# Performance work log

Measured on AMD Instinct MI355X. Metric: run time of the kernel, lower is better.

The kernel has to match this reference:

```python
import jax, jax.numpy as jnp
import numpy as np

N, E = 50000, 1600000
F_IN, EDGE_DIM, HID, HEADS, NCLS = 64, 16, 128, 4, 40
C = HID // HEADS  # per-head dim = 32


def setup_inputs() -> dict:
    key = jax.random.key(0)
    ks = jax.random.split(key, 20)
    s = 0.1
    inp = {
        'x': jax.random.normal(ks[0], (N, F_IN), jnp.float32),
        'edge_index': jax.random.randint(ks[1], (2, E), 0, N, jnp.int64),
        'edge_attr': jax.random.normal(ks[2], (E, EDGE_DIM), jnp.float32),
        # layer 1 params
        'W1': jax.random.normal(ks[3], (HID, F_IN), jnp.float32) * s,
        'as1': jax.random.normal(ks[4], (HEADS, C), jnp.float32) * s,
        'ad1': jax.random.normal(ks[5], (HEADS, C), jnp.float32) * s,
        'ae1': jax.random.normal(ks[6], (HEADS, C), jnp.float32) * s,
        'We1': jax.random.normal(ks[7], (HID, EDGE_DIM), jnp.float32) * s,
        'b1': jnp.zeros((HID,), jnp.float32),
        # layer 2 params
        'W2': jax.random.normal(ks[8], (HID, HID), jnp.float32) * s,
        'as2': jax.random.normal(ks[9], (HEADS, C), jnp.float32) * s,
        'ad2': jax.random.normal(ks[10], (HEADS, C), jnp.float32) * s,
        'ae2': jax.random.normal(ks[11], (HEADS, C), jnp.float32) * s,
        'We2': jax.random.normal(ks[12], (HID, EDGE_DIM), jnp.float32) * s,
        'b2': jnp.zeros((HID,), jnp.float32),
        # final classifier
        'Wlin': jax.random.normal(ks[13], (NCLS, HID), jnp.float32) * s,
        'blin': jnp.zeros((NCLS,), jnp.float32),
    }
    return inp


def gat_conv(x, src, dst, eattr, W, a_s, a_d, a_e, We, b):
    """PyG GATConv (concat=True, add_self_loops=True, fill_value='mean'), eval mode."""
    n = x.shape[0]
    H, Cd = a_s.shape
    h = (x @ W.T).reshape(n, H, Cd)  # [N,H,C]
    # self-loop edge_attr = per-destination mean of incoming edge_attr
    cnt = jax.ops.segment_sum(jnp.ones((dst.shape[0],), eattr.dtype), dst, num_segments=n)
    mean_ea = jax.ops.segment_sum(eattr, dst, num_segments=n) / jnp.maximum(cnt, 1.0)[:, None]
    loops = jnp.arange(n, dtype=src.dtype)
    s_idx = jnp.concatenate([src, loops])
    d_idx = jnp.concatenate([dst, loops])
    ea = jnp.concatenate([eattr, mean_ea], axis=0)  # [E+N, edge_dim]
    e = (ea @ We.T).reshape(-1, H, Cd)
    # edge-wise attention logits
    alpha = (h * a_s).sum(-1)[s_idx] + (h * a_d).sum(-1)[d_idx] + (e * a_e).sum(-1)  # [E+N,H]
    alpha = jax.nn.leaky_relu(alpha, 0.2)
    # segment softmax over destination neighborhoods (every node has a self-loop)
    amax = jax.ops.segment_max(alpha, d_idx, num_segments=n)
    ex = jnp.exp(alpha - amax[d_idx])
    den = jax.ops.segment_sum(ex, d_idx, num_segments=n)
    coef = ex / (den[d_idx] + 1e-16)
    out = jax.ops.segment_sum(h[s_idx] * coef[:, :, None], d_idx, num_segments=n)
    return out.reshape(n, H * Cd) + b


def reference(x, edge_index, edge_attr, W1, as1, ad1, ae1, We1, b1,
              W2, as2, ad2, ae2, We2, b2, Wlin, blin):
    src, dst = edge_index[0], edge_index[1]
    h = jax.nn.relu(gat_conv(x, src, dst, edge_attr, W1, as1, ad1, ae1, We1, b1))
    h = jax.nn.relu(gat_conv(h, src, dst, edge_attr, W2, as2, ad2, ae2, We2, b2))
    logits = h @ Wlin.T + blin
    return jax.nn.log_softmax(logits, axis=1)
```

## Files before the change

### kernel.cpp

```cpp
#include <hip/hip_runtime.h>
#include <hip/hip_bf16.h>
#include <math.h>


#define CHUNK 2048

typedef __attribute__((ext_vector_type(8))) short short8;
typedef __attribute__((ext_vector_type(4))) float floatx4;
typedef __attribute__((ext_vector_type(2))) float floatx2;

__device__ __forceinline__ unsigned short f2bf(float f) {
  unsigned u = __float_as_uint(f);
  unsigned r = u + 0x7FFFu + ((u >> 16) & 1u);
  return (unsigned short)(r >> 16);
}
__device__ __forceinline__ float bf2f(unsigned short b) {
  return __uint_as_float(((unsigned)b) << 16);
}

__global__ __launch_bounds__(256) void alphaseq_kernel(const float* __restrict__ ea,
                                                       const float* __restrict__ ae1,
                                                       const float* __restrict__ We1,
                                                       const float* __restrict__ ae2,
                                                       const float* __restrict__ We2,
                                                       const int* __restrict__ dst,
                                                       int* __restrict__ bucketCnt,
                                                       uint2* __restrict__ tA1,
                                                       uint2* __restrict__ tA2,
                                                       int E, int NB) {
  __shared__ float wa[128];
  __shared__ int hist[512];
  const int tid = threadIdx.x;
  hist[tid] = 0;
  hist[tid + 256] = 0;
  if (tid < 128) {
    const float* aev = (tid < 64) ? ae1 : ae2;
    const float* Wev = (tid < 64) ? We1 : We2;
    const int h = (tid >> 4) & 3;
    const int d = tid & 15;
    float s = 0.f;
#pragma unroll
    for (int c = 0; c < 32; ++c) s += aev[h * 32 + c] * Wev[(h * 32 + c) * 16 + d];
    wa[tid] = s;
  }
  __syncthreads();
  const int e0 = blockIdx.x * CHUNK, e1 = min(e0 + CHUNK, E);
  for (int e = e0 + tid; e < e1; e += 256) {
    atomicAdd(&hist[dst[e] >> 7], 1);
    const float4* p = (const float4*)(ea + (size_t)e * 16);
    float4 q0 = p[0], q1 = p[1], q2 = p[2], q3 = p[3];
    float v[16] = {q0.x, q0.y, q0.z, q0.w, q1.x, q1.y, q1.z, q1.w,
                   q2.x, q2.y, q2.z, q2.w, q3.x, q3.y, q3.z, q3.w};
    unsigned short rr[8];
#pragma unroll
    for (int h = 0; h < 8; ++h) {
      float s = 0.f;
#pragma unroll
      for (int d = 0; d < 16; ++d) s += v[d] * wa[h * 16 + d];
      rr[h] = f2bf(s);
    }
    uint2 lo, hi;
    lo.x = ((unsigned)rr[1] << 16) | rr[0];
    lo.y = ((unsigned)rr[3] << 16) | rr[2];
    hi.x = ((unsigned)rr[5] << 16) | rr[4];
    hi.y = ((unsigned)rr[7] << 16) | rr[6];
    tA1[e] = lo;
    tA2[e] = hi;
  }
  __syncthreads();
  for (int i = tid; i < NB; i += 256)
    if (hist[i]) atomicAdd(&bucketCnt[i], hist[i]);
}

__global__ __launch_bounds__(512) void scanB_kernel(const int* __restrict__ bucketCnt,
                                                    int* __restrict__ bucketOffs,
                                                    int* __restrict__ bucketPos,
                                                    int* __restrict__ offs,
                                                    int NB, int N, int E) {
  __shared__ int sc[512];
  const int tid = threadIdx.x;
  const int v = (tid < NB) ? bucketCnt[tid] : 0;
  sc[tid] = v;
  __syncthreads();
  for (int off = 1; off < 512; off <<= 1) {
    int t = (tid >= off) ? sc[tid - off] : 0;
    __syncthreads();
    sc[tid] += t;
    __syncthreads();
  }
  const int excl = sc[tid] - v;
  if (tid < NB) { bucketOffs[tid] = excl; bucketPos[tid] = excl; }
  if (tid == 0) { bucketOffs[NB] = E; offs[N] = E; }
}

__global__ __launch_bounds__(512) void partB_kernel(const int* __restrict__ src,
                                                    const int* __restrict__ dst,
                                                    const uint2* __restrict__ tA1,
                                                    const uint2* __restrict__ tA2,
                                                    int* __restrict__ bucketPos,
                                                    int4* __restrict__ binned16,
                                                    int* __restrict__ binned4,
                                                    unsigned char* __restrict__ dlArr,
                                                    int E, int NB) {
  __shared__ int hist[512], sc[512], lbase[513], gbase[512], lcnt[512];
  __shared__ int4 stg16[CHUNK];
  __shared__ int stg4[CHUNK];
  __shared__ unsigned char stg1[CHUNK];
  const int tid = threadIdx.x;
  const int e0 = blockIdx.x * CHUNK;
  const int e1 = min(e0 + CHUNK, E);
  hist[tid] = 0; lcnt[tid] = 0;
  __syncthreads();
  for (int e = e0 + tid; e < e1; e += 512) atomicAdd(&hist[dst[e] >> 7], 1);
  __syncthreads();
  sc[tid] = hist[tid];
  __syncthreads();
  for (int off = 1; off < 512; off <<= 1) {
    int t = (tid >= off) ? sc[tid - off] : 0;
    __syncthreads();
    sc[tid] += t;
    __syncthreads();
  }
  lbase[tid + 1] = sc[tid];
  if (tid == 0) lbase[0] = 0;
  if (tid < NB && hist[tid] > 0) gbase[tid] = atomicAdd(&bucketPos[tid], hist[tid]);
  __syncthreads();
  for (int e = e0 + tid; e < e1; e += 512) {
    const int d = dst[e];
    const int b = d >> 7;
    const int lr = atomicAdd(&lcnt[b], 1);
    const uint2 a1 = tA1[e];
    const uint2 a2 = tA2[e];
    int4 v;
    v.x = (src[e] & 0xFFFF) | ((d & 127) << 16);
    v.y = (int)a1.x;
    v.z = (int)a1.y;
    v.w = (int)a2.x;
    const int sp = lbase[b] + lr;
    stg16[sp] = v;
    stg4[sp] = (int)a2.y;
    stg1[sp] = (unsigned char)(d & 127);
  }
  __syncthreads();
  const int total = e1 - e0;
  for (int t = tid; t < total; t += 512) {
    int lo = 0, hi = 511;
    while (lo < hi) {
      int mid = (lo + hi + 1) >> 1;
      if (lbase[mid] <= t) lo = mid; else hi = mid - 1;
    }
    const int g = gbase[lo] + (t - lbase[lo]);
    binned16[g] = stg16[t];
    binned4[g] = stg4[t];
    dlArr[g] = stg1[t];
  }
}

__global__ __launch_bounds__(256) void passC_kernel(const int4* __restrict__ binned16,
                                                    const int* __restrict__ binned4,
                                                    const unsigned char* __restrict__ dlArr,
                                                    const int* __restrict__ bucketOffs,
                                                    int* __restrict__ srcS,
                                                    uint2* __restrict__ aeS1,
                                                    uint2* __restrict__ aeS2,
                                                    int* __restrict__ offs, int N) {
  __shared__ int cnt[128], dbase[129], dpos[128];
  const int tid = threadIdx.x;
  const int b = blockIdx.x;
  const int bo = bucketOffs[b], be = bucketOffs[b + 1];
  const int m = be - bo;
  if (tid < 128) { cnt[tid] = 0; dpos[tid] = 0; }
  __syncthreads();
  for (int t = tid; t < m; t += 256) atomicAdd(&cnt[dlArr[bo + t]], 1);
  __syncthreads();
  for (int off = 1; off < 128; off <<= 1) {
    int t = (tid < 128 && tid >= (unsigned)off) ? cnt[tid - off] : 0;
    __syncthreads();
    if (tid < 128) cnt[tid] += t;
    __syncthreads();
  }
  if (tid == 0) dbase[0] = 0;
  if (tid < 128) dbase[tid + 1] = cnt[tid];
  __syncthreads();
  const int dcnt = min(128, N - (b << 7));
  if (tid < dcnt) offs[(b << 7) + tid] = bo + dbase[tid];
  for (int t = tid; t < m; t += 256) {
    const int4 v = binned16[bo + t];
    const int w4 = binned4[bo + t];
    const int dl = (v.x >> 16) & 127;
    const int p = dbase[dl] + atomicAdd(&dpos[dl], 1);
    srcS[bo + p] = v.x & 0xFFFF;
    aeS1[bo + p] = make_uint2((unsigned)v.y, (unsigned)v.z);
    aeS2[bo + p] = make_uint2((unsigned)v.w, (unsigned)w4);
  }
}

__global__ __launch_bounds__(256) void cvtall_kernel(const float* __restrict__ W1,
                                                     unsigned short* __restrict__ Wb1,
                                                     const float* __restrict__ W2,
                                                     unsigned short* __restrict__ Wb2,
                                                     const float* __restrict__ Wlin,
                                                     unsigned short* __restrict__ whi,
                                                     unsigned short* __restrict__ wlo) {
  const int n1 = 128 * 64, n2 = 128 * 128, n3 = 48 * 128;
  int i = blockIdx.x * 256 + threadIdx.x;
  if (i < n1) {
    Wb1[i] = f2bf(W1[i]);
  } else if (i < n1 + n2) {
    Wb2[i - n1] = f2bf(W2[i - n1]);
  } else if (i < n1 + n2 + n3) {
    const int j = i - n1 - n2;
    float v = (j < 40 * 128) ? Wlin[j] : 0.f;
    unsigned short h = f2bf(v);
    whi[j] = h;
    wlo[j] = f2bf(v - bf2f(h));
  }
}

#define GEMM_SCORE_EPILOGUE()                                                      \
  {                                                                                \
    const float as0 = a_s[ncol0], as1v = a_s[ncol0 + 16];                          \
    const float ad0 = a_d[ncol0], ad1v = a_d[ncol0 + 16];                          \
    _Pragma("unroll") for (int mt = 0; mt < 4; ++mt) {                             \
      _Pragma("unroll") for (int r = 0; r < 4; ++r) {                              \
        float ps = acc[mt][0][r] * as0 + acc[mt][1][r] * as1v;                     \
        float pd = acc[mt][0][r] * ad0 + acc[mt][1][r] * ad1v;                     \
        _Pragma("unroll") for (int off = 8; off; off >>= 1) {                      \
          ps += __shfl_xor(ps, off, 16);                                           \
          pd += __shfl_xor(pd, off, 16);                                           \
        }                                                                          \
        if (l15 == 0) {                                                            \
          const int row = m0 + mt * 16 + (quad << 2) + r;                          \
          if (row < n) {                                                           \
            ssc[(size_t)row * 4 + w] = ps;                                         \
            dsc[(size_t)row * 4 + w] = pd;                                         \
          }                                                                        \
        }                                                                          \
      }                                                                            \
    }                                                                              \
  }

__global__ __launch_bounds__(256) void gemm_score_f32_kernel(const float* __restrict__ X,
                                                             const unsigned short* __restrict__ Wb,
                                                             const float* __restrict__ a_s,
                                                             const float* __restrict__ a_d,
                                                             unsigned short* __restrict__ H,
                                                             float* __restrict__ ssc,
                                                             float* __restrict__ dsc,
                                                             int n) {
  const int w = threadIdx.x >> 6;
  const int lane = threadIdx.x & 63;
  const int m0 = blockIdx.x * 64;
  const int quad = lane >> 4;
  const int l15 = lane & 15;
  floatx4 acc[4][2];
#pragma unroll
  for (int mt = 0; mt < 4; ++mt)
#pragma unroll
    for (int nt = 0; nt < 2; ++nt) acc[mt][nt] = (floatx4)(0.f);

  int rowm[4];
#pragma unroll
  for (int mt = 0; mt < 4; ++mt) {
    int r = m0 + mt * 16 + l15;
    rowm[mt] = (r < n) ? r : (n - 1);
  }
  const int ncol0 = (w << 5) + l15;

#pragma unroll
  for (int kc = 0; kc < 64; kc += 32) {
    const int koff = kc + (quad << 3);
    short8 a[4], b[2];
#pragma unroll
    for (int mt = 0; mt < 4; ++mt) {
      const float* pr = X + (size_t)rowm[mt] * 64 + koff;
      float4 q0 = *(const float4*)pr;
      float4 q1 = *(const float4*)(pr + 4);
      a[mt][0] = (short)f2bf(q0.x); a[mt][1] = (short)f2bf(q0.y);
      a[mt][2] = (short)f2bf(q0.z); a[mt][3] = (short)f2bf(q0.w);
      a[mt][4] = (short)f2bf(q1.x); a[mt][5] = (short)f2bf(q1.y);
      a[mt][6] = (short)f2bf(q1.z); a[mt][7] = (short)f2bf(q1.w);
    }
#pragma unroll
    for (int nt = 0; nt < 2; ++nt)
      b[nt] = *(const short8*)(Wb + (size_t)(ncol0 + nt * 16) * 64 + koff);
#pragma unroll
    for (int mt = 0; mt < 4; ++mt)
#pragma unroll
      for (int nt = 0; nt < 2; ++nt)
        acc[mt][nt] = __builtin_amdgcn_mfma_f32_16x16x32_bf16(a[mt], b[nt], acc[mt][nt], 0, 0, 0);
  }
#pragma unroll
  for (int mt = 0; mt < 4; ++mt) {
    const int rbase = m0 + mt * 16 + (quad << 2);
#pragma unroll
    for (int nt = 0; nt < 2; ++nt) {
      const int col = ncol0 + nt * 16;
#pragma unroll
      for (int r = 0; r < 4; ++r) {
        const int row = rbase + r;
        if (row < n) H[(size_t)row * 128 + col] = f2bf(acc[mt][nt][r]);
      }
    }
  }
  GEMM_SCORE_EPILOGUE()
}

__global__ __launch_bounds__(256) void gemm_score_kernel(const unsigned short* __restrict__ X,
                                                         const unsigned short* __restrict__ Wb,
                                                         const float* __restrict__ a_s,
                                                         const float* __restrict__ a_d,
                                                         unsigned short* __restrict__ H,
                                                         float* __restrict__ ssc,
                                                         float* __restrict__ dsc,
                                                         int n, int K) {
  const int w = threadIdx.x >> 6;
  const int lane = threadIdx.x & 63;
  const int m0 = blockIdx.x * 64;
  const int quad = lane >> 4;
  const int l15 = lane & 15;
  floatx4 acc[4][2];
#pragma unroll
  for (int mt = 0; mt < 4; ++mt)
#pragma unroll
    for (int nt = 0; nt < 2; ++nt) acc[mt][nt] = (floatx4)(0.f);

  int rowm[4];
#pragma unroll
  for (int mt = 0; mt < 4; ++mt) {
    int r = m0 + mt * 16 + l15;
    rowm[mt] = (r < n) ? r : (n - 1);
  }
  const int ncol0 = (w << 5) + l15;

  for (int kc = 0; kc < K; kc += 32) {
    const int koff = kc + (quad << 3);
    short8 a[4], b[2];
#pragma unroll
    for (int mt = 0; mt < 4; ++mt)
      a[mt] = *(const short8*)(X + (size_t)rowm[mt] * K + koff);
#pragma unroll
    for (int nt = 0; nt < 2; ++nt)
      b[nt] = *(const short8*)(Wb + (size_t)(ncol0 + nt * 16) * K + koff);
#pragma unroll
    for (int mt = 0; mt < 4; ++mt)
#pragma unroll
      for (int nt = 0; nt < 2; ++nt)
        acc[mt][nt] = __builtin_amdgcn_mfma_f32_16x16x32_bf16(a[mt], b[nt], acc[mt][nt], 0, 0, 0);
  }
#pragma unroll
  for (int mt = 0; mt < 4; ++mt) {
    const int rbase = m0 + mt * 16 + (quad << 2);
#pragma unroll
    for (int nt = 0; nt < 2; ++nt) {
      const int col = ncol0 + nt * 16;
#pragma unroll
      for (int r = 0; r < 4; ++r) {
        const int row = rbase + r;
        if (row < n) H[(size_t)row * 128 + col] = f2bf(acc[mt][nt][r]);
      }
    }
  }
  GEMM_SCORE_EPILOGUE()
}

__device__ __forceinline__ float leaky02(float a) { return a > 0.f ? a : 0.2f * a; }
__device__ __forceinline__ float sel4(float4 v, int h) {
  return (h == 0) ? v.x : (h == 1) ? v.y : (h == 2) ? v.z : v.w;
}

__global__ __launch_bounds__(256) void agg_kernel(const unsigned short* __restrict__ hin,
                                                  const float* __restrict__ ssc,
                                                  const float* __restrict__ dsc,
                                                  const unsigned short* __restrict__ aeS,
                                                  const int* __restrict__ offs,
                                                  const int* __restrict__ srcS,
                                                  const float* __restrict__ bias,
                                                  unsigned short* __restrict__ hout, int n) {
  __shared__ int sbuf[4][64];
  __shared__ float pbuf[4][256];
  const int tid = threadIdx.x;
  const int wv = tid >> 6;
  const int lane = tid & 63;
  const int node = blockIdx.x * 4 + wv;
  if (node >= n) return;
  const int l32 = lane & 31;
  const int half = lane >> 5;
  const int ch4 = l32 * 4;
  const int headB = l32 >> 3;
  const float4 dv = *(const float4*)(dsc + (size_t)node * 4);
  float4 l4 = make_float4(0.f, 0.f, 0.f, 0.f);
  float4 sa = make_float4(0.f, 0.f, 0.f, 0.f);
  floatx2 acc01 = (floatx2)(0.f);
  floatx2 acc23 = (floatx2)(0.f);
  const int j0 = offs[node], j1 = offs[node + 1];

  for (int jc = j0; jc < j1; jc += 64) {
    const int len = min(64, j1 - jc);
    float4 p4 = make_float4(0.f, 0.f, 0.f, 0.f);
    int sv = 0;
    if (lane < len) {
      const int j = jc + lane;
      sv = srcS[j];
      const ushort4 aq = *(const ushort4*)(aeS + (size_t)j * 4);
      const float4 ae4 = make_float4(bf2f(aq.x), bf2f(aq.y), bf2f(aq.z), bf2f(aq.w));
      const float4 ss4 = *(const float4*)(ssc + (size_t)sv * 4);
      sa.x += ae4.x; sa.y += ae4.y; sa.z += ae4.z; sa.w += ae4.w;
      p4.x = __expf(leaky02(ss4.x + dv.x + ae4.x));
      p4.y = __expf(leaky02(ss4.y + dv.y + ae4.y));
      p4.z = __expf(leaky02(ss4.z + dv.z + ae4.z));
      p4.w = __expf(leaky02(ss4.w + dv.w + ae4.w));
    }
    sbuf[wv][lane] = sv;
    *(float4*)(&pbuf[wv][lane * 4]) = p4;
    l4.x += p4.x; l4.y += p4.y; l4.z += p4.z; l4.w += p4.w;
    int k = 0;
    for (; k + 8 <= len; k += 8) {
      int s[4];
      float p[4];
      uint2 d[4];
#pragma unroll
      for (int u = 0; u < 4; ++u) {
        const int kk = k + 2 * u + half;
        s[u] = sbuf[wv][kk];
        p[u] = pbuf[wv][kk * 4 + headB];
      }
#pragma unroll
      for (int u = 0; u < 4; ++u)
        d[u] = *(const uint2*)(hin + (size_t)s[u] * 128 + ch4);
#pragma unroll
      for (int u = 0; u < 4; ++u) {
        floatx2 p2; p2.x = p[u]; p2.y = p[u];
        floatx2 h01, h23;
        h01.x = __uint_as_float(d[u].x << 16);
        h01.y = __uint_as_float(d[u].x & 0xFFFF0000u);
        h23.x = __uint_as_float(d[u].y << 16);
        h23.y = __uint_as_float(d[u].y & 0xFFFF0000u);
        acc01 += p2 * h01;
        acc23 += p2 * h23;
      }
    }
    for (; k < len; k += 2) {
      int kk = k + half;
      if (kk < len) {
        int s = sbuf[wv][kk];
        float p = pbuf[wv][kk * 4 + headB];
        uint2 d = *(const uint2*)(hin + (size_t)s * 128 + ch4);
        floatx2 p2; p2.x = p; p2.y = p;
        floatx2 h01, h23;
        h01.x = __uint_as_float(d.x << 16);
        h01.y = __uint_as_float(d.x & 0xFFFF0000u);
        h23.x = __uint_as_float(d.y << 16);
        h23.y = __uint_as_float(d.y & 0xFFFF0000u);
        acc01 += p2 * h01;
        acc23 += p2 * h23;
      }
    }
  }

  float acc[4] = {acc01.x, acc01.y, acc23.x, acc23.y};
#pragma unroll
  for (int off = 32; off; off >>= 1) {
    sa.x += __shfl_xor(sa.x, off);
    sa.y += __shfl_xor(sa.y, off);
    sa.z += __shfl_xor(sa.z, off);
    sa.w += __shfl_xor(sa.w, off);
    l4.x += __shfl_xor(l4.x, off);
    l4.y += __shfl_xor(l4.y, off);
    l4.z += __shfl_xor(l4.z, off);
    l4.w += __shfl_xor(l4.w, off);
  }
#pragma unroll
  for (int i = 0; i < 4; ++i) acc[i] += __shfl_xor(acc[i], 32);

  const int deg = j1 - j0;
  const float invd = 1.f / fmaxf((float)deg, 1.f);
  const float ssn = ssc[(size_t)node * 4 + headB];
  const float aloop = leaky02(ssn + sel4(dv, headB) + sel4(sa, headB) * invd);
  const float pl = __expf(aloop);
  const float lF = sel4(l4, headB) + pl;
  const uint2 hd = *(const uint2*)(hin + (size_t)node * 128 + ch4);
  const float hv0 = __uint_as_float(hd.x << 16);
  const float hv1 = __uint_as_float(hd.x & 0xFFFF0000u);
  const float hv2 = __uint_as_float(hd.y << 16);
  const float hv3 = __uint_as_float(hd.y & 0xFFFF0000u);
  const float inv = 1.f / (lF + 1e-16f);
  const float4 bi = *(const float4*)(bias + ch4);
  const float o0 = fmaxf((acc[0] + pl * hv0) * inv + bi.x, 0.f);
  const float o1 = fmaxf((acc[1] + pl * hv1) * inv + bi.y, 0.f);
  const float o2 = fmaxf((acc[2] + pl * hv2) * inv + bi.z, 0.f);
  const float o3 = fmaxf((acc[3] + pl * hv3) * inv + bi.w, 0.f);
  if (half == 0) {
    ushort4 o;
    o.x = f2bf(o0); o.y = f2bf(o1); o.z = f2bf(o2); o.w = f2bf(o3);
    *(ushort4*)(hout + (size_t)node * 128 + ch4) = o;
  }
}

__global__ __launch_bounds__(256) void classifier_kernel(const unsigned short* __restrict__ h,
                                                         const unsigned short* __restrict__ Whi,
                                                         const unsigned short* __restrict__ Wlo,
                                                         const float* __restrict__ blin,
                                                         float* __restrict__ out, int n) {
  const int w = threadIdx.x >> 6;
  const int lane = threadIdx.x & 63;
  const int quad = lane >> 4;
  const int l15 = lane & 15;
  const int row0 = blockIdx.x * 64 + w * 16;
  if (row0 >= n) return;
  int rowm = row0 + l15;
  if (rowm >= n) rowm = n - 1;
  floatx4 acc[3];
#pragma unroll
  for (int nt = 0; nt < 3; ++nt) acc[nt] = (floatx4)(0.f);
  const size_t hbase = (size_t)rowm * 128;
#pragma unroll
  for (int kc = 0; kc < 128; kc += 32) {
    const int koff = kc + (quad << 3);
    short8 a = *(const short8*)(h + hbase + koff);
#pragma unroll
    for (int nt = 0; nt < 3; ++nt) {
      short8 bh = *(const short8*)(Whi + (size_t)(nt * 16 + l15) * 128 + koff);
      short8 bl = *(const short8*)(Wlo + (size_t)(nt * 16 + l15) * 128 + koff);
      acc[nt] = __builtin_amdgcn_mfma_f32_16x16x32_bf16(a, bh, acc[nt], 0, 0, 0);
      acc[nt] = __builtin_amdgcn_mfma_f32_16x16x32_bf16(a, bl, acc[nt], 0, 0, 0);
    }
  }
  const float bl0 = blin[l15];
  const float bl1 = blin[16 + l15];
  const float bl2 = (l15 < 8) ? blin[32 + l15] : 0.f;
#pragma unroll
  for (int r = 0; r < 4; ++r) {
    const int rrow = row0 + (quad << 2) + r;
    const float v0 = acc[0][r] + bl0;
    const float v1 = acc[1][r] + bl1;
    const float v2 = (l15 < 8) ? (acc[2][r] + bl2) : -INFINITY;
    float m = fmaxf(v0, fmaxf(v1, v2));
#pragma unroll
    for (int off = 8; off; off >>= 1) m = fmaxf(m, __shfl_xor(m, off, 16));
    const float e2 = (l15 < 8) ? __expf(v2 - m) : 0.f;
    float s = __expf(v0 - m) + __expf(v1 - m) + e2;
#pragma unroll
    for (int off = 8; off; off >>= 1) s += __shfl_xor(s, off, 16);
    const float ls = m + __logf(s);
    if (rrow < n) {
      float* po = out + (size_t)rrow * 40;
      po[l15] = v0 - ls;
      po[16 + l15] = v1 - ls;
      if (l15 < 8) po[32 + l15] = v2 - ls;
    }
  }
}

extern "C" void kernel_launch(void* const* d_in, const int* in_sizes, int n_in,
                              void* d_out, int out_size, void* d_ws, size_t ws_size,
                              hipStream_t stream) {
  const float* x    = (const float*)d_in[0];
  const int*   eidx = (const int*)d_in[1];
  const float* ea   = (const float*)d_in[2];
  const float* W1   = (const float*)d_in[3];
  const float* as1  = (const float*)d_in[4];
  const float* ad1  = (const float*)d_in[5];
  const float* ae1w = (const float*)d_in[6];
  const float* We1  = (const float*)d_in[7];
  const float* b1   = (const float*)d_in[8];
  const float* W2   = (const float*)d_in[9];
  const float* as2  = (const float*)d_in[10];
  const float* ad2  = (const float*)d_in[11];
  const float* ae2w = (const float*)d_in[12];
  const float* We2  = (const float*)d_in[13];
  const float* b2   = (const float*)d_in[14];
  const float* Wlin = (const float*)d_in[15];
  const float* blin = (const float*)d_in[16];
  float* out = (float*)d_out;

  const int N = in_sizes[0] / 64;
  const int E = in_sizes[1] / 2;
  const int* src = eidx;
  const int* dst = eidx + E;
  const int NB = (N + 127) >> 7;

  char* wsb = (char*)d_ws;
  size_t off = 0;
  auto alloc = [&](size_t bytes) -> void* {
    void* p = wsb + off;
    off = (off + bytes + 255) & ~(size_t)255;
    return p;
  };
  int* bucketCnt  = (int*)alloc(512 * 4);
  int* bucketOffs = (int*)alloc(513 * 4);
  int* bucketPos  = (int*)alloc(512 * 4);
  int* offs       = (int*)alloc((size_t)(N + 1) * 4);
  uint2* tA1      = (uint2*)alloc((size_t)E * 8);
  uint2* tA2      = (uint2*)alloc((size_t)E * 8);
  void* regC      = alloc((size_t)E * 16);
  int4* binned16  = (int4*)regC;
  unsigned short* hA = (unsigned short*)regC;
  int* binned4    = (int*)alloc((size_t)E * 4);
  unsigned char* dlArr = (unsigned char*)alloc((size_t)E);
  int* srcS       = (int*)alloc((size_t)E * 4);
  unsigned short* Wb1 = (unsigned short*)alloc(128 * 64 * 2);
  unsigned short* Wb2 = (unsigned short*)alloc(128 * 128 * 2);
  unsigned short* Wlh = (unsigned short*)alloc(48 * 128 * 2);
  unsigned short* Wll = (unsigned short*)alloc(48 * 128 * 2);
  float* ssc      = (float*)alloc((size_t)N * 4 * 4);
  float* dsc      = (float*)alloc((size_t)N * 4 * 4);
  unsigned short* hB = (unsigned short*)alloc((size_t)N * 128 * 2);
  uint2* aeS1 = tA1;
  uint2* aeS2 = tA2;

  const int gg = (N + 63) / 64;
  const int gs = (N + 3) / 4;
  const int gp = (E + CHUNK - 1) / CHUNK;
  const int ncvt = 128 * 64 + 128 * 128 + 48 * 128;

  hipMemsetAsync(bucketCnt, 0, 512 * 4, stream);
  alphaseq_kernel<<<gp, 256, 0, stream>>>(ea, ae1w, We1, ae2w, We2, dst, bucketCnt,
                                          tA1, tA2, E, NB);
  scanB_kernel<<<1, 512, 0, stream>>>(bucketCnt, bucketOffs, bucketPos, offs, NB, N, E);
  partB_kernel<<<gp, 512, 0, stream>>>(src, dst, tA1, tA2, bucketPos, binned16, binned4,
                                       dlArr, E, NB);
  passC_kernel<<<NB, 256, 0, stream>>>(binned16, binned4, dlArr, bucketOffs, srcS,
                                       aeS1, aeS2, offs, N);

  cvtall_kernel<<<(ncvt + 255) / 256, 256, 0, stream>>>(W1, Wb1, W2, Wb2, Wlin, Wlh, Wll);

  gemm_score_f32_kernel<<<gg, 256, 0, stream>>>(x, Wb1, as1, ad1, hA, ssc, dsc, N);
  agg_kernel<<<gs, 256, 0, stream>>>(hA, ssc, dsc, (const unsigned short*)aeS1, offs, srcS, b1, hB, N);

  gemm_score_kernel<<<gg, 256, 0, stream>>>(hB, Wb2, as2, ad2, hA, ssc, dsc, N, 128);
  agg_kernel<<<gs, 256, 0, stream>>>(hA, ssc, dsc, (const unsigned short*)aeS2, offs, srcS, b2, hB, N);

  classifier_kernel<<<gg, 256, 0, stream>>>(hB, Wlh, Wll, blin, out, N);
}
```

Before: 473.5 us.

## Stage GEMM tiles in LDS and scatter partB directly without local staging

The two score GEMM kernels now cooperatively load the A row tile and the full weight matrix into padded LDS before running the MFMA loop, instead of each lane issuing strided global loads per k-step. The fp32 input is converted to bf16 once during staging. Separately, partB drops its block-local prefix scan, shared staging buffers and binary-search copy-out, writing each edge straight to its global bucket slot. That saves LDS and synchronisation but makes the global writes scattered and uncoalesced, and edge order within a bucket now depends on atomic timing.

```diff
diff --git a/kernel.cpp b/kernel.cpp
--- a/kernel.cpp
+++ b/kernel.cpp
@@ -102,10 +102,7 @@
                                                     int* __restrict__ binned4,
                                                     unsigned char* __restrict__ dlArr,
                                                     int E, int NB) {
-  __shared__ int hist[512], sc[512], lbase[513], gbase[512], lcnt[512];
-  __shared__ int4 stg16[CHUNK];
-  __shared__ int stg4[CHUNK];
-  __shared__ unsigned char stg1[CHUNK];
+  __shared__ int hist[512], gbase[512], lcnt[512];
   const int tid = threadIdx.x;
   const int e0 = blockIdx.x * CHUNK;
   const int e1 = min(e0 + CHUNK, E);
@@ -113,22 +110,13 @@
   __syncthreads();
   for (int e = e0 + tid; e < e1; e += 512) atomicAdd(&hist[dst[e] >> 7], 1);
   __syncthreads();
-  sc[tid] = hist[tid];
-  __syncthreads();
-  for (int off = 1; off < 512; off <<= 1) {
-    int t = (tid >= off) ? sc[tid - off] : 0;
-    __syncthreads();
-    sc[tid] += t;
-    __syncthreads();
-  }
-  lbase[tid + 1] = sc[tid];
-  if (tid == 0) lbase[0] = 0;
   if (tid < NB && hist[tid] > 0) gbase[tid] = atomicAdd(&bucketPos[tid], hist[tid]);
   __syncthreads();
   for (int e = e0 + tid; e < e1; e += 512) {
     const int d = dst[e];
     const int b = d >> 7;
     const int lr = atomicAdd(&lcnt[b], 1);
+    const int g = gbase[b] + lr;
     const uint2 a1 = tA1[e];
     const uint2 a2 = tA2[e];
     int4 v;
@@ -136,23 +124,9 @@
     v.y = (int)a1.x;
     v.z = (int)a1.y;
     v.w = (int)a2.x;
-    const int sp = lbase[b] + lr;
-    stg16[sp] = v;
-    stg4[sp] = (int)a2.y;
-    stg1[sp] = (unsigned char)(d & 127);
-  }
-  __syncthreads();
-  const int total = e1 - e0;
-  for (int t = tid; t < total; t += 512) {
-    int lo = 0, hi = 511;
-    while (lo < hi) {
-      int mid = (lo + hi + 1) >> 1;
-      if (lbase[mid] <= t) lo = mid; else hi = mid - 1;
-    }
-    const int g = gbase[lo] + (t - lbase[lo]);
-    binned16[g] = stg16[t];
-    binned4[g] = stg4[t];
-    dlArr[g] = stg1[t];
+    binned16[g] = v;
+    binned4[g] = (int)a2.y;
+    dlArr[g] = (unsigned char)(d & 127);
   }
 }
 
@@ -240,6 +214,37 @@
     }                                                                              \
   }
 
+#define GEMM_MFMA_FROM_LDS(KTOT, PA, PB)                                           \
+  {                                                                                \
+    for (int kc = 0; kc < (KTOT); kc += 32) {                                      \
+      const int koff = kc + (quad << 3);                                           \
+      short8 a[4], b[2];                                                           \
+      _Pragma("unroll") for (int mt = 0; mt < 4; ++mt)                             \
+        a[mt] = *(const short8*)(&As[(mt * 16 + l15) * (PA) + koff]);              \
+      _Pragma("unroll") for (int nt = 0; nt < 2; ++nt)                             \
+        b[nt] = *(const short8*)(&Bs[(ncol0 + nt * 16) * (PB) + koff]);            \
+      _Pragma("unroll") for (int mt = 0; mt < 4; ++mt)                             \
+        _Pragma("unroll") for (int nt = 0; nt < 2; ++nt)                           \
+          acc[mt][nt] =                                                            \
+              __builtin_amdgcn_mfma_f32_16x16x32_bf16(a[mt], b[nt], acc[mt][nt],   \
+                                                      0, 0, 0);                    \
+    }                                                                              \
+  }
+
+#define GEMM_WRITE_H()                                                             \
+  {                                                                                \
+    _Pragma("unroll") for (int mt = 0; mt < 4; ++mt) {                             \
+      const int rbase = m0 + mt * 16 + (quad << 2);                                \
+      _Pragma("unroll") for (int nt = 0; nt < 2; ++nt) {                           \
+        const int col = ncol0 + nt * 16;                                           \
+        _Pragma("unroll") for (int r = 0; r < 4; ++r) {                            \
+          const int row = rbase + r;                                               \
+          if (row < n) H[(size_t)row * 128 + col] = f2bf(acc[mt][nt][r]);          \
+        }                                                                          \
+      }                                                                            \
+    }                                                                              \
+  }
+
 __global__ __launch_bounds__(256) void gemm_score_f32_kernel(const float* __restrict__ X,
                                                              const unsigned short* __restrict__ Wb,
                                                              const float* __restrict__ a_s,
@@ -248,61 +253,44 @@
                                                              float* __restrict__ ssc,
                                                              float* __restrict__ dsc,
                                                              int n) {
-  const int w = threadIdx.x >> 6;
-  const int lane = threadIdx.x & 63;
+  __shared__ unsigned short As[64 * 72];
+  __shared__ unsigned short Bs[128 * 72];
+  const int tid = threadIdx.x;
+  const int w = tid >> 6;
+  const int lane = tid & 63;
   const int m0 = blockIdx.x * 64;
   const int quad = lane >> 4;
   const int l15 = lane & 15;
+
+#pragma unroll
+  for (int it = 0; it < 4; ++it) {
+    const int idx = it * 256 + tid;
+    const int row = idx >> 4;
+    const int c4 = (idx & 15) * 4;
+    const int grow = min(m0 + row, n - 1);
+    const float4 q = *(const float4*)(X + (size_t)grow * 64 + c4);
+    unsigned short* dstp = &As[row * 72 + c4];
+    dstp[0] = f2bf(q.x); dstp[1] = f2bf(q.y); dstp[2] = f2bf(q.z); dstp[3] = f2bf(q.w);
+  }
+#pragma unroll
+  for (int it = 0; it < 4; ++it) {
+    const int idx = it * 256 + tid;
+    const int row = idx >> 3;
+    const int c8 = (idx & 7) * 8;
+    short8 v = *(const short8*)(Wb + (size_t)row * 64 + c8);
+    *(short8*)(&Bs[row * 72 + c8]) = v;
+  }
+  __syncthreads();
+
   floatx4 acc[4][2];
 #pragma unroll
   for (int mt = 0; mt < 4; ++mt)
 #pragma unroll
     for (int nt = 0; nt < 2; ++nt) acc[mt][nt] = (floatx4)(0.f);
-
-  int rowm[4];
-#pragma unroll
-  for (int mt = 0; mt < 4; ++mt) {
-    int r = m0 + mt * 16 + l15;
-    rowm[mt] = (r < n) ? r : (n - 1);
-  }
   const int ncol0 = (w << 5) + l15;
 
-#pragma unroll
-  for (int kc = 0; kc < 64; kc += 32) {
-    const int koff = kc + (quad << 3);
-    short8 a[4], b[2];
-#pragma unroll
-    for (int mt = 0; mt < 4; ++mt) {
-      const float* pr = X + (size_t)rowm[mt] * 64 + koff;
-      float4 q0 = *(const float4*)pr;
-      float4 q1 = *(const float4*)(pr + 4);
-      a[mt][0] = (short)f2bf(q0.x); a[mt][1] = (short)f2bf(q0.y);
-      a[mt][2] = (short)f2bf(q0.z); a[mt][3] = (short)f2bf(q0.w);
-      a[mt][4] = (short)f2bf(q1.x); a[mt][5] = (short)f2bf(q1.y);
-      a[mt][6] = (short)f2bf(q1.z); a[mt][7] = (short)f2bf(q1.w);
-    }
-#pragma unroll
-    for (int nt = 0; nt < 2; ++nt)
-      b[nt] = *(const short8*)(Wb + (size_t)(ncol0 + nt * 16) * 64 + koff);
-#pragma unroll
-    for (int mt = 0; mt < 4; ++mt)
-#pragma unroll
-      for (int nt = 0; nt < 2; ++nt)
-        acc[mt][nt] = __builtin_amdgcn_mfma_f32_16x16x32_bf16(a[mt], b[nt], acc[mt][nt], 0, 0, 0);
-  }
-#pragma unroll
-  for (int mt = 0; mt < 4; ++mt) {
-    const int rbase = m0 + mt * 16 + (quad << 2);
-#pragma unroll
-    for (int nt = 0; nt < 2; ++nt) {
-      const int col = ncol0 + nt * 16;
-#pragma unroll
-      for (int r = 0; r < 4; ++r) {
-        const int row = rbase + r;
-        if (row < n) H[(size_t)row * 128 + col] = f2bf(acc[mt][nt][r]);
-      }
-    }
-  }
+  GEMM_MFMA_FROM_LDS(64, 72, 72)
+  GEMM_WRITE_H()
   GEMM_SCORE_EPILOGUE()
 }
 
@@ -313,54 +301,44 @@
                                                          unsigned short* __restrict__ H,
                                                          float* __restrict__ ssc,
                                                          float* __restrict__ dsc,
-                                                         int n, int K) {
-  const int w = threadIdx.x >> 6;
-  const int lane = threadIdx.x & 63;
+                                                         int n) {
+  __shared__ unsigned short As[64 * 136];
+  __shared__ unsigned short Bs[128 * 136];
+  const int tid = threadIdx.x;
+  const int w = tid >> 6;
+  const int lane = tid & 63;
   const int m0 = blockIdx.x * 64;
   const int quad = lane >> 4;
   const int l15 = lane & 15;
+
+#pragma unroll
+  for (int it = 0; it < 4; ++it) {
+    const int idx = it * 256 + tid;
+    const int row = idx >> 4;
+    const int c8 = (idx & 15) * 8;
+    const int grow = min(m0 + row, n - 1);
+    short8 v = *(const short8*)(X + (size_t)grow * 128 + c8);
+    *(short8*)(&As[row * 136 + c8]) = v;
+  }
+#pragma unroll
+  for (int it = 0; it < 8; ++it) {
+    const int idx = it * 256 + tid;
+    const int row = idx >> 4;
+    const int c8 = (idx & 15) * 8;
+    short8 v = *(const short8*)(Wb + (size_t)row * 128 + c8);
+    *(short8*)(&Bs[row * 136 + c8]) = v;
+  }
+  __syncthreads();
+
   floatx4 acc[4][2];
 #pragma unroll
   for (int mt = 0; mt < 4; ++mt)
 #pragma unroll
     for (int nt = 0; nt < 2; ++nt) acc[mt][nt] = (floatx4)(0.f);
-
-  int rowm[4];
-#pragma unroll
-  for (int mt = 0; mt < 4; ++mt) {
-    int r = m0 + mt * 16 + l15;
-    rowm[mt] = (r < n) ? r : (n - 1);
-  }
   const int ncol0 = (w << 5) + l15;
 
-  for (int kc = 0; kc < K; kc += 32) {
-    const int koff = kc + (quad << 3);
-    short8 a[4], b[2];
-#pragma unroll
-    for (int mt = 0; mt < 4; ++mt)
-      a[mt] = *(const short8*)(X + (size_t)rowm[mt] * K + koff);
-#pragma unroll
-    for (int nt = 0; nt < 2; ++nt)
-      b[nt] = *(const short8*)(Wb + (size_t)(ncol0 + nt * 16) * K + koff);
-#pragma unroll
-    for (int mt = 0; mt < 4; ++mt)
-#pragma unroll
-      for (int nt = 0; nt < 2; ++nt)
-        acc[mt][nt] = __builtin_amdgcn_mfma_f32_16x16x32_bf16(a[mt], b[nt], acc[mt][nt], 0, 0, 0);
-  }
-#pragma unroll
-  for (int mt = 0; mt < 4; ++mt) {
-    const int rbase = m0 + mt * 16 + (quad << 2);
-#pragma unroll
-    for (int nt = 0; nt < 2; ++nt) {
-      const int col = ncol0 + nt * 16;
-#pragma unroll
-      for (int r = 0; r < 4; ++r) {
-        const int row = rbase + r;
-        if (row < n) H[(size_t)row * 128 + col] = f2bf(acc[mt][nt][r]);
-      }
-    }
-  }
+  GEMM_MFMA_FROM_LDS(128, 136, 136)
+  GEMM_WRITE_H()
   GEMM_SCORE_EPILOGUE()
 }
 
@@ -628,7 +606,7 @@
   gemm_score_f32_kernel<<<gg, 256, 0, stream>>>(x, Wb1, as1, ad1, hA, ssc, dsc, N);
   agg_kernel<<<gs, 256, 0, stream>>>(hA, ssc, dsc, (const unsigned short*)aeS1, offs, srcS, b1, hB, N);
 
-  gemm_score_kernel<<<gg, 256, 0, stream>>>(hB, Wb2, as2, ad2, hA, ssc, dsc, N, 128);
+  gemm_score_kernel<<<gg, 256, 0, stream>>>(hB, Wb2, as2, ad2, hA, ssc, dsc, N);
   agg_kernel<<<gs, 256, 0, stream>>>(hA, ssc, dsc, (const unsigned short*)aeS2, offs, srcS, b2, hB, N);
 
   classifier_kernel<<<gg, 256, 0, stream>>>(hB, Wlh, Wll, blin, out, N);
```

New measurement: 491.6 us. 1.04x slower.
